# Performance work log

Measured on AMD Instinct MI355X. Metric: run time of the kernel, lower is better.

## Reference

```python
import jax, jax.numpy as jnp
import numpy as np

N, E, DIN, H, C = 50000, 800000, 256, 128, 8


def setup_inputs() -> dict:
    key = jax.random.key(0)
    k1, k2, k3, k4 = jax.random.split(key, 4)
    x = jax.random.normal(k1, (N, DIN), dtype=jnp.float32)
    edge_index = jax.random.randint(k2, (2, E), 0, N, dtype=jnp.int64)
    W1 = jax.random.normal(k3, (DIN, H), dtype=jnp.float32) * (1.0 / np.sqrt(DIN))
    b1 = jnp.zeros((H,), dtype=jnp.float32)
    W2 = jax.random.normal(k4, (H, C), dtype=jnp.float32) * (1.0 / np.sqrt(H))
    b2 = jnp.zeros((C,), dtype=jnp.float32)
    return {"x": x, "W1": W1, "b1": b1, "W2": W2, "b2": b2, "edge_index": edge_index}


def reference(x, W1, b1, W2, b2, edge_index):
    n = x.shape[0]
    loop = jnp.arange(n, dtype=edge_index.dtype)
    src = jnp.concatenate([edge_index[0], loop])  # messages flow src -> dst
    dst = jnp.concatenate([edge_index[1], loop])
    # symmetric GCN normalization with self-loops (PyG GCNConv default)
    deg = jax.ops.segment_sum(jnp.ones_like(dst, dtype=x.dtype), dst, num_segments=n)
    dinv = jnp.where(deg > 0, deg ** -0.5, 0.0)
    norm = dinv[src] * dinv[dst]  # [E+N]

    def gcn_layer(h, W, b):
        h = h @ W                                   # [N, d_out]
        msg = norm[:, None] * h[src]                # gather: [E+N, d_out]
        agg = jax.ops.segment_sum(msg, dst, num_segments=n)  # scatter-add
        return agg + b

    h = jax.nn.relu(gcn_layer(x, W1, b1))
    # F.dropout(training=False) is identity in eval mode
    out = gcn_layer(h, W2, b2)
    return jax.nn.log_softmax(out, axis=1)
```

## Files before the change

kernel.cpp:

```cpp
#include <hip/hip_runtime.h>
#include <hip/hip_bf16.h>
#include <hip/hip_fp16.h>
#include <stdint.h>

#define DIN 256
#define HD  128
#define CD  8
#define KCH 64
#define SBW 72
#define CSRW 64

typedef __attribute__((ext_vector_type(8))) short bf16x8;
typedef __attribute__((ext_vector_type(4))) float f32x4;

__device__ __forceinline__ float bf2f(unsigned short u) {
    union { unsigned int i; float f; } v; v.i = ((unsigned int)u) << 16; return v.f;
}
__device__ __forceinline__ unsigned short f2bf(float f) {
    union { float f; unsigned int i; } v; v.f = f;
    unsigned int r = v.i + 0x7fffu + ((v.i >> 16) & 1u);
    return (unsigned short)(r >> 16);
}
__device__ __forceinline__ int edge_at(const void* ei, int is64, long long idx) {
    return is64 ? (int)((const long long*)ei)[idx] : ((const int*)ei)[idx];
}

__global__ __launch_bounds__(256) void prep_kernel(
    const float* __restrict__ W1, unsigned short* __restrict__ W1T,
    int* __restrict__ count, int N)
{
    int tg = blockIdx.x * 256 + threadIdx.x;
    if (tg < HD * (DIN / 4)) {
        int n  = tg & (HD - 1);
        int k4 = (tg >> 7) * 4;
        unsigned short v[4];
#pragma unroll
        for (int j = 0; j < 4; j++) v[j] = f2bf(W1[(k4 + j) * HD + n]);
        *reinterpret_cast<unsigned long long*>(W1T + (size_t)n * DIN + k4) =
            ((unsigned long long)v[0]) | ((unsigned long long)v[1] << 16) |
            ((unsigned long long)v[2] << 32) | ((unsigned long long)v[3] << 48);
    }
    for (int i = tg; i < N; i += 256 * 256) count[i] = 0;
}

__global__ __launch_bounds__(256) void gemm1_scatter_kernel(
    const float* __restrict__ x, const unsigned short* __restrict__ W1T,
    unsigned short* __restrict__ h, int M,
    const void* __restrict__ ei,
    int* __restrict__ count, unsigned short* __restrict__ colf, int E, int N, int G1)
{
    __shared__ unsigned short w1t[HD * SBW];
    if ((int)blockIdx.x >= G1) {
        const int lane = threadIdx.x & 63;
        int oddw = ((const int*)ei)[2 * lane + 1];
        unsigned long long zb = __ballot(oddw == 0);
        int is64 = (__popcll(zb) >= 56) ? 1 : 0;
        int e0 = ((int)blockIdx.x - G1) * 512 + threadIdx.x;
#pragma unroll
        for (int k = 0; k < 2; k++) {
            int e = e0 + k * 256;
            if (e < E) {
                int s = edge_at(ei, is64, e);
                int d = edge_at(ei, is64, (long long)E + e);
                if ((unsigned)d < (unsigned)N && (unsigned)s < (unsigned)N) {
                    int slot = atomicAdd(&count[d], 1);
                    if (slot < CSRW)
                        colf[(d << 6) + slot] = (unsigned short)s;
                }
            }
        }
        return;
    }
    const int tid  = threadIdx.x;
    const int lane = tid & 63;
    const int wave = tid >> 6;
    const int quad = lane >> 4;
    const int r15  = lane & 15;
    const long long rowBase = (long long)blockIdx.x * 128 + wave * 32;

    f32x4 acc[2][8];
#pragma unroll
    for (int rt = 0; rt < 2; rt++)
#pragma unroll
        for (int ct = 0; ct < 8; ct++)
#pragma unroll
            for (int i = 0; i < 4; i++) acc[rt][ct][i] = 0.0f;

    for (int kh = 0; kh < DIN / KCH; kh++) {
        __syncthreads();
        for (int c = tid; c < HD * (KCH / 8); c += 256) {
            int n   = c >> 3;
            int kk0 = (c & 7) * 8;
            bf16x8 v = *reinterpret_cast<const bf16x8*>(W1T + (size_t)n * DIN + kh * KCH + kk0);
            *reinterpret_cast<bf16x8*>(&w1t[n * SBW + kk0]) = v;
        }
        __syncthreads();

        for (int ki = 0; ki < KCH / 32; ki++) {
            int kk0 = ki * 32 + quad * 8;
            int kg  = kh * KCH + kk0;
            bf16x8 a[2];
#pragma unroll
            for (int rt = 0; rt < 2; rt++) {
                long long row = rowBase + rt * 16 + r15;
                if (row < M) {
                    const float* xp = x + row * DIN + kg;
                    f32x4 f0 = *reinterpret_cast<const f32x4*>(xp);
                    f32x4 f1 = *reinterpret_cast<const f32x4*>(xp + 4);
#pragma unroll
                    for (int j = 0; j < 4; j++) {
                        a[rt][j]     = (short)f2bf(f0[j]);
                        a[rt][j + 4] = (short)f2bf(f1[j]);
                    }
                } else {
#pragma unroll
                    for (int j = 0; j < 8; j++) a[rt][j] = 0;
                }
            }
#pragma unroll
            for (int ct = 0; ct < 8; ct++) {
                bf16x8 b = *reinterpret_cast<const bf16x8*>(&w1t[(ct * 16 + r15) * SBW + kk0]);
                acc[0][ct] = __builtin_amdgcn_mfma_f32_16x16x32_bf16(a[0], b, acc[0][ct], 0, 0, 0);
                acc[1][ct] = __builtin_amdgcn_mfma_f32_16x16x32_bf16(a[1], b, acc[1][ct], 0, 0, 0);
            }
        }
    }
#pragma unroll
    for (int rt = 0; rt < 2; rt++)
#pragma unroll
        for (int ct = 0; ct < 8; ct++)
#pragma unroll
            for (int i = 0; i < 4; i++) {
                long long row = rowBase + rt * 16 + quad * 4 + i;
                if (row < M) h[row * HD + ct * 16 + r15] = f2bf(acc[rt][ct][i]);
            }
}

__global__ __launch_bounds__(256) void scale_kernel(
    const unsigned short* __restrict__ h, const int* __restrict__ count,
    unsigned short* __restrict__ h2, int N)
{
    int t = blockIdx.x * 256 + threadIdx.x;
    if (t >= N * (HD / 8)) return;
    int n = t >> 4;
    int deg = count[n]; if (deg > CSRW) deg = CSRW;
    float dn = rsqrtf((float)deg + 1.0f);
    bf16x8 v = *reinterpret_cast<const bf16x8*>(h + (size_t)t * 8);
    bf16x8 o;
#pragma unroll
    for (int j = 0; j < 8; j++) {
        float f = bf2f((unsigned short)v[j]) * dn;
        __half hf = __float2half(f);
        o[j] = *reinterpret_cast<short*>(&hf);
    }
    *reinterpret_cast<bf16x8*>(h2 + (size_t)t * 8) = o;
}

__global__ __launch_bounds__(256) void agg1_fused_kernel(
    const unsigned short* __restrict__ h2, const int* __restrict__ count,
    const unsigned short* __restrict__ colf, const float* __restrict__ b1,
    const float* __restrict__ W2, float* __restrict__ hw2, int N)
{
    const int lane = threadIdx.x & 63;
    const int n = blockIdx.x * 4 + (threadIdx.x >> 6);
    if (n >= N) return;

    float w2a[CD], w2b[CD];
#pragma unroll
    for (int c = 0; c < CD; c++) {
        w2a[c] = W2[(2 * lane)     * CD + c];
        w2b[c] = W2[(2 * lane + 1) * CD + c];
    }

    int deg = count[n]; if (deg > CSRW) deg = CSRW;
    const float dn = rsqrtf((float)deg + 1.0f);

    union UH { unsigned int u; __half2 h; };
    UH p; p.u = *reinterpret_cast<const unsigned int*>(h2 + ((size_t)n << 7) + 2 * lane);
    float2 pf = __half22float2(p.h);
    float acc0 = pf.x, acc1 = pf.y;

    const int base = n << 6;
    int i = 0;
    for (; i + 7 < deg; i += 8) {
        unsigned long long c0 = *reinterpret_cast<const unsigned long long*>(colf + base + i);
        unsigned long long c1 = *reinterpret_cast<const unsigned long long*>(colf + base + i + 4);
        unsigned int s[8];
#pragma unroll
        for (int j = 0; j < 4; j++) {
            s[j]     = (unsigned int)((c0 >> (16 * j)) & 0xFFFFu);
            s[j + 4] = (unsigned int)((c1 >> (16 * j)) & 0xFFFFu);
        }
        UH hv[8];
#pragma unroll
        for (int j = 0; j < 8; j++)
            hv[j].u = *reinterpret_cast<const unsigned int*>(h2 + ((size_t)s[j] << 7) + 2 * lane);
#pragma unroll
        for (int j = 0; j < 8; j++) {
            float2 f = __half22float2(hv[j].h);
            acc0 += f.x;
            acc1 += f.y;
        }
    }
    for (; i < deg; i++) {
        unsigned int s0 = colf[base + i];
        UH a; a.u = *reinterpret_cast<const unsigned int*>(h2 + ((size_t)s0 << 7) + 2 * lane);
        float2 f = __half22float2(a.h);
        acc0 += f.x;
        acc1 += f.y;
    }

    float v0 = dn * acc0 + b1[2 * lane];     v0 = v0 > 0.0f ? v0 : 0.0f;
    float v1 = dn * acc1 + b1[2 * lane + 1]; v1 = v1 > 0.0f ? v1 : 0.0f;

    float part[CD];
#pragma unroll
    for (int c = 0; c < CD; c++) part[c] = v0 * w2a[c] + v1 * w2b[c];

    float t4[4];
    {
        int hi = lane & 1;
#pragma unroll
        for (int k = 0; k < 4; k++) {
            float send = hi ? part[k] : part[4 + k];
            float recv = __shfl_xor(send, 1, 64);
            t4[k] = (hi ? part[4 + k] : part[k]) + recv;
        }
    }
    float t2[2];
    {
        int hi = (lane >> 1) & 1;
#pragma unroll
        for (int k = 0; k < 2; k++) {
            float send = hi ? t4[k] : t4[2 + k];
            float recv = __shfl_xor(send, 2, 64);
            t2[k] = (hi ? t4[2 + k] : t4[k]) + recv;
        }
    }
    float t1;
    {
        int hi = (lane >> 2) & 1;
        float send = hi ? t2[0] : t2[1];
        float recv = __shfl_xor(send, 4, 64);
        t1 = (hi ? t2[1] : t2[0]) + recv;
    }
    t1 += __shfl_xor(t1, 8, 64);
    t1 += __shfl_xor(t1, 16, 64);
    t1 += __shfl_xor(t1, 32, 64);
    int c = ((lane & 1) << 2) | (lane & 2) | ((lane >> 2) & 1);
    if (lane < CD) hw2[(size_t)n * CD + c] = dn * t1;
}

__global__ __launch_bounds__(256) void agg2_kernel(
    const float* __restrict__ hw2, const int* __restrict__ count,
    const unsigned short* __restrict__ colf, const float* __restrict__ b2,
    float* __restrict__ out, int N) {
    int n = blockIdx.x * 256 + threadIdx.x;
    if (n >= N) return;
    int deg = count[n]; if (deg > CSRW) deg = CSRW;
    float dn = rsqrtf((float)deg + 1.0f);
    f32x4 a0 = *reinterpret_cast<const f32x4*>(hw2 + (size_t)n * CD);
    f32x4 a1 = *reinterpret_cast<const f32x4*>(hw2 + (size_t)n * CD + 4);
    const int base = n << 6;
    int i = 0;
    for (; i + 3 < deg; i += 4) {
        unsigned long long cc = *reinterpret_cast<const unsigned long long*>(colf + base + i);
        unsigned int s0 = (unsigned int)(cc & 0xFFFFu);
        unsigned int s1 = (unsigned int)((cc >> 16) & 0xFFFFu);
        unsigned int s2 = (unsigned int)((cc >> 32) & 0xFFFFu);
        unsigned int s3 = (unsigned int)((cc >> 48) & 0xFFFFu);
        f32x4 b0 = *reinterpret_cast<const f32x4*>(hw2 + (size_t)s0 * CD);
        f32x4 b1 = *reinterpret_cast<const f32x4*>(hw2 + (size_t)s0 * CD + 4);
        f32x4 c0 = *reinterpret_cast<const f32x4*>(hw2 + (size_t)s1 * CD);
        f32x4 c1 = *reinterpret_cast<const f32x4*>(hw2 + (size_t)s1 * CD + 4);
        f32x4 d0 = *reinterpret_cast<const f32x4*>(hw2 + (size_t)s2 * CD);
        f32x4 d1 = *reinterpret_cast<const f32x4*>(hw2 + (size_t)s2 * CD + 4);
        f32x4 e0 = *reinterpret_cast<const f32x4*>(hw2 + (size_t)s3 * CD);
        f32x4 e1 = *reinterpret_cast<const f32x4*>(hw2 + (size_t)s3 * CD + 4);
        a0 += (b0 + c0) + (d0 + e0);
        a1 += (b1 + c1) + (d1 + e1);
    }
    for (; i < deg; i++) {
        unsigned int s0 = colf[base + i];
        a0 += *reinterpret_cast<const f32x4*>(hw2 + (size_t)s0 * CD);
        a1 += *reinterpret_cast<const f32x4*>(hw2 + (size_t)s0 * CD + 4);
    }
    float v[CD];
#pragma unroll
    for (int j = 0; j < 4; j++) {
        v[j]     = dn * a0[j] + b2[j];
        v[4 + j] = dn * a1[j] + b2[4 + j];
    }
    float mx = v[0];
#pragma unroll
    for (int j = 1; j < CD; j++) mx = fmaxf(mx, v[j]);
    float s8 = 0.0f;
#pragma unroll
    for (int j = 0; j < CD; j++) s8 += expf(v[j] - mx);
    float lse = mx + logf(s8);
    f32x4 o0, o1;
#pragma unroll
    for (int j = 0; j < 4; j++) {
        o0[j] = v[j] - lse;
        o1[j] = v[4 + j] - lse;
    }
    *reinterpret_cast<f32x4*>(out + (size_t)n * CD)     = o0;
    *reinterpret_cast<f32x4*>(out + (size_t)n * CD + 4) = o1;
}

extern "C" void kernel_launch(void* const* d_in, const int* in_sizes, int n_in,
                              void* d_out, int out_size, void* d_ws, size_t ws_size,
                              hipStream_t stream) {
    const float* x  = (const float*)d_in[0];
    const float* W1 = (const float*)d_in[1];
    const float* b1 = (const float*)d_in[2];
    const float* W2 = (const float*)d_in[3];
    const float* b2 = (const float*)d_in[4];
    const void*  ei = d_in[5];
    const int N = in_sizes[0] / DIN;
    const int E = in_sizes[5] / 2;
    const int G1 = (N + 127) / 128;
    const int G2 = (E + 511) / 512;

    char* ws = (char*)d_ws;
    size_t off = 0;
    auto alloc = [&](size_t bytes) -> void* {
        void* p = ws + off;
        off = (off + bytes + 255) & ~(size_t)255;
        return p;
    };
    int*   count = (int*)alloc((size_t)N * 4);
    unsigned short* colf = (unsigned short*)alloc((size_t)N * CSRW * 2);
    unsigned short* h = (unsigned short*)alloc((size_t)N * HD * 2);
    unsigned short* h2 = (unsigned short*)alloc((size_t)N * HD * 2);
    float* hw2 = (float*)alloc((size_t)N * CD * 4);
    unsigned short* W1T = (unsigned short*)alloc((size_t)HD * DIN * 2);

    prep_kernel         <<<256, 256, 0, stream>>>(W1, W1T, count, N);
    gemm1_scatter_kernel<<<G1 + G2, 256, 0, stream>>>(x, W1T, h, N, ei, count, colf, E, N, G1);
    scale_kernel        <<<(N * (HD / 8) + 255) / 256, 256, 0, stream>>>(h, count, h2, N);
    agg1_fused_kernel   <<<(N + 3) / 4, 256, 0, stream>>>(h2, count, colf, b1, W2, hw2, N);
    agg2_kernel         <<<(N + 255) / 256, 256, 0, stream>>>(hw2, count, colf, b2,
                                                              (float*)d_out, N);
}
```

Measured before the change: 195.7 us.

## Pad degree counters and split agg1 gather across two half-wave edge streams

```diff
diff --git a/kernel.cpp b/kernel.cpp
--- a/kernel.cpp
+++ b/kernel.cpp
@@ -9,6 +9,7 @@
 #define KCH 64
 #define SBW 72
 #define CSRW 64
+#define CPAD 8
 
 typedef __attribute__((ext_vector_type(8))) short bf16x8;
 typedef __attribute__((ext_vector_type(4))) float f32x4;
@@ -40,7 +41,7 @@
             ((unsigned long long)v[0]) | ((unsigned long long)v[1] << 16) |
             ((unsigned long long)v[2] << 32) | ((unsigned long long)v[3] << 48);
     }
-    for (int i = tg; i < N; i += 256 * 256) count[i] = 0;
+    for (int i = tg; i < N * CPAD; i += 256 * 256) count[i] = 0;
 }
 
 __global__ __launch_bounds__(256) void gemm1_scatter_kernel(
@@ -63,7 +64,7 @@
                 int s = edge_at(ei, is64, e);
                 int d = edge_at(ei, is64, (long long)E + e);
                 if ((unsigned)d < (unsigned)N && (unsigned)s < (unsigned)N) {
-                    int slot = atomicAdd(&count[d], 1);
+                    int slot = atomicAdd(&count[(size_t)d * CPAD], 1);
                     if (slot < CSRW)
                         colf[(d << 6) + slot] = (unsigned short)s;
                 }
@@ -143,7 +144,7 @@
     int t = blockIdx.x * 256 + threadIdx.x;
     if (t >= N * (HD / 8)) return;
     int n = t >> 4;
-    int deg = count[n]; if (deg > CSRW) deg = CSRW;
+    int deg = count[(size_t)n * CPAD]; if (deg > CSRW) deg = CSRW;
     float dn = rsqrtf((float)deg + 1.0f);
     bf16x8 v = *reinterpret_cast<const bf16x8*>(h + (size_t)t * 8);
     bf16x8 o;
@@ -162,60 +163,86 @@
     const float* __restrict__ W2, float* __restrict__ hw2, int N)
 {
     const int lane = threadIdx.x & 63;
+    const int half = lane >> 5;
+    const int l32  = lane & 31;
     const int n = blockIdx.x * 4 + (threadIdx.x >> 6);
     if (n >= N) return;
 
-    float w2a[CD], w2b[CD];
-#pragma unroll
-    for (int c = 0; c < CD; c++) {
-        w2a[c] = W2[(2 * lane)     * CD + c];
-        w2b[c] = W2[(2 * lane + 1) * CD + c];
-    }
-
-    int deg = count[n]; if (deg > CSRW) deg = CSRW;
+    f32x4 w2lo[4], w2hi[4];
+#pragma unroll
+    for (int k = 0; k < 4; k++) {
+        w2lo[k] = *reinterpret_cast<const f32x4*>(W2 + (4 * l32 + k) * CD);
+        w2hi[k] = *reinterpret_cast<const f32x4*>(W2 + (4 * l32 + k) * CD + 4);
+    }
+
+    int deg = count[(size_t)n * CPAD]; if (deg > CSRW) deg = CSRW;
     const float dn = rsqrtf((float)deg + 1.0f);
 
-    union UH { unsigned int u; __half2 h; };
-    UH p; p.u = *reinterpret_cast<const unsigned int*>(h2 + ((size_t)n << 7) + 2 * lane);
-    float2 pf = __half22float2(p.h);
-    float acc0 = pf.x, acc1 = pf.y;
+    union UH4 { uint2 u; __half2 h[2]; };
+    float a0 = 0.0f, a1 = 0.0f, a2 = 0.0f, a3 = 0.0f;
+    if (half == 0) {
+        UH4 p; p.u = *reinterpret_cast<const uint2*>(h2 + ((size_t)n << 7) + 4 * l32);
+        float2 f0 = __half22float2(p.h[0]), f1 = __half22float2(p.h[1]);
+        a0 = f0.x; a1 = f0.y; a2 = f1.x; a3 = f1.y;
+    }
 
     const int base = n << 6;
+    const int sh = 16 * half;
     int i = 0;
     for (; i + 7 < deg; i += 8) {
         unsigned long long c0 = *reinterpret_cast<const unsigned long long*>(colf + base + i);
         unsigned long long c1 = *reinterpret_cast<const unsigned long long*>(colf + base + i + 4);
-        unsigned int s[8];
-#pragma unroll
-        for (int j = 0; j < 4; j++) {
-            s[j]     = (unsigned int)((c0 >> (16 * j)) & 0xFFFFu);
-            s[j + 4] = (unsigned int)((c1 >> (16 * j)) & 0xFFFFu);
-        }
-        UH hv[8];
-#pragma unroll
-        for (int j = 0; j < 8; j++)
-            hv[j].u = *reinterpret_cast<const unsigned int*>(h2 + ((size_t)s[j] << 7) + 2 * lane);
-#pragma unroll
-        for (int j = 0; j < 8; j++) {
-            float2 f = __half22float2(hv[j].h);
-            acc0 += f.x;
-            acc1 += f.y;
-        }
-    }
-    for (; i < deg; i++) {
-        unsigned int s0 = colf[base + i];
-        UH a; a.u = *reinterpret_cast<const unsigned int*>(h2 + ((size_t)s0 << 7) + 2 * lane);
-        float2 f = __half22float2(a.h);
-        acc0 += f.x;
-        acc1 += f.y;
-    }
-
-    float v0 = dn * acc0 + b1[2 * lane];     v0 = v0 > 0.0f ? v0 : 0.0f;
-    float v1 = dn * acc1 + b1[2 * lane + 1]; v1 = v1 > 0.0f ? v1 : 0.0f;
-
+        unsigned int s0 = (unsigned int)((c0 >> sh) & 0xFFFFu);
+        unsigned int s1 = (unsigned int)((c0 >> (32 + sh)) & 0xFFFFu);
+        unsigned int s2 = (unsigned int)((c1 >> sh) & 0xFFFFu);
+        unsigned int s3 = (unsigned int)((c1 >> (32 + sh)) & 0xFFFFu);
+        UH4 v0, v1, v2, v3;
+        v0.u = *reinterpret_cast<const uint2*>(h2 + ((size_t)s0 << 7) + 4 * l32);
+        v1.u = *reinterpret_cast<const uint2*>(h2 + ((size_t)s1 << 7) + 4 * l32);
+        v2.u = *reinterpret_cast<const uint2*>(h2 + ((size_t)s2 << 7) + 4 * l32);
+        v3.u = *reinterpret_cast<const uint2*>(h2 + ((size_t)s3 << 7) + 4 * l32);
+#pragma unroll
+        for (int j = 0; j < 1; j++) {}
+        {
+            float2 f;
+            f = __half22float2(v0.h[0]); a0 += f.x; a1 += f.y;
+            f = __half22float2(v0.h[1]); a2 += f.x; a3 += f.y;
+            f = __half22float2(v1.h[0]); a0 += f.x; a1 += f.y;
+            f = __half22float2(v1.h[1]); a2 += f.x; a3 += f.y;
+            f = __half22float2(v2.h[0]); a0 += f.x; a1 += f.y;
+            f = __half22float2(v2.h[1]); a2 += f.x; a3 += f.y;
+            f = __half22float2(v3.h[0]); a0 += f.x; a1 += f.y;
+            f = __half22float2(v3.h[1]); a2 += f.x; a3 += f.y;
+        }
+    }
+    for (; i + 1 < deg; i += 2) {
+        unsigned int s = colf[base + i + half];
+        UH4 v; v.u = *reinterpret_cast<const uint2*>(h2 + ((size_t)s << 7) + 4 * l32);
+        float2 f0 = __half22float2(v.h[0]), f1 = __half22float2(v.h[1]);
+        a0 += f0.x; a1 += f0.y; a2 += f1.x; a3 += f1.y;
+    }
+    if (i < deg && half == 0) {
+        unsigned int s = colf[base + i];
+        UH4 v; v.u = *reinterpret_cast<const uint2*>(h2 + ((size_t)s << 7) + 4 * l32);
+        float2 f0 = __half22float2(v.h[0]), f1 = __half22float2(v.h[1]);
+        a0 += f0.x; a1 += f0.y; a2 += f1.x; a3 += f1.y;
+    }
+
+    a0 += __shfl_xor(a0, 32, 64);
+    a1 += __shfl_xor(a1, 32, 64);
+    a2 += __shfl_xor(a2, 32, 64);
+    a3 += __shfl_xor(a3, 32, 64);
+
+    float v0 = dn * a0 + b1[4 * l32];     v0 = v0 > 0.0f ? v0 : 0.0f;
+    float v1 = dn * a1 + b1[4 * l32 + 1]; v1 = v1 > 0.0f ? v1 : 0.0f;
+    float v2 = dn * a2 + b1[4 * l32 + 2]; v2 = v2 > 0.0f ? v2 : 0.0f;
+    float v3 = dn * a3 + b1[4 * l32 + 3]; v3 = v3 > 0.0f ? v3 : 0.0f;
+
+    f32x4 plo = v0 * w2lo[0] + v1 * w2lo[1] + v2 * w2lo[2] + v3 * w2lo[3];
+    f32x4 phi = v0 * w2hi[0] + v1 * w2hi[1] + v2 * w2hi[2] + v3 * w2hi[3];
     float part[CD];
 #pragma unroll
-    for (int c = 0; c < CD; c++) part[c] = v0 * w2a[c] + v1 * w2b[c];
+    for (int c = 0; c < 4; c++) { part[c] = plo[c]; part[4 + c] = phi[c]; }
 
     float t4[4];
     {
@@ -246,7 +273,6 @@
     }
     t1 += __shfl_xor(t1, 8, 64);
     t1 += __shfl_xor(t1, 16, 64);
-    t1 += __shfl_xor(t1, 32, 64);
     int c = ((lane & 1) << 2) | (lane & 2) | ((lane >> 2) & 1);
     if (lane < CD) hw2[(size_t)n * CD + c] = dn * t1;
 }
@@ -257,7 +283,7 @@
     float* __restrict__ out, int N) {
     int n = blockIdx.x * 256 + threadIdx.x;
     if (n >= N) return;
-    int deg = count[n]; if (deg > CSRW) deg = CSRW;
+    int deg = count[(size_t)n * CPAD]; if (deg > CSRW) deg = CSRW;
     float dn = rsqrtf((float)deg + 1.0f);
     f32x4 a0 = *reinterpret_cast<const f32x4*>(hw2 + (size_t)n * CD);
     f32x4 a1 = *reinterpret_cast<const f32x4*>(hw2 + (size_t)n * CD + 4);
@@ -270,7 +296,7 @@
         unsigned int s2 = (unsigned int)((cc >> 32) & 0xFFFFu);
         unsigned int s3 = (unsigned int)((cc >> 48) & 0xFFFFu);
         f32x4 b0 = *reinterpret_cast<const f32x4*>(hw2 + (size_t)s0 * CD);
-        f32x4 b1 = *reinterpret_cast<const f32x4*>(hw2 + (size_t)s0 * CD + 4);
+        f32x4 b1v = *reinterpret_cast<const f32x4*>(hw2 + (size_t)s0 * CD + 4);
         f32x4 c0 = *reinterpret_cast<const f32x4*>(hw2 + (size_t)s1 * CD);
         f32x4 c1 = *reinterpret_cast<const f32x4*>(hw2 + (size_t)s1 * CD + 4);
         f32x4 d0 = *reinterpret_cast<const f32x4*>(hw2 + (size_t)s2 * CD);
@@ -278,7 +304,7 @@
         f32x4 e0 = *reinterpret_cast<const f32x4*>(hw2 + (size_t)s3 * CD);
         f32x4 e1 = *reinterpret_cast<const f32x4*>(hw2 + (size_t)s3 * CD + 4);
         a0 += (b0 + c0) + (d0 + e0);
-        a1 += (b1 + c1) + (d1 + e1);
+        a1 += (b1v + c1) + (d1 + e1);
     }
     for (; i < deg; i++) {
         unsigned int s0 = colf[base + i];
@@ -329,7 +355,7 @@
         off = (off + bytes + 255) & ~(size_t)255;
         return p;
     };
-    int*   count = (int*)alloc((size_t)N * 4);
+    int*   count = (int*)alloc((size_t)N * CPAD * 4);
     unsigned short* colf = (unsigned short*)alloc((size_t)N * CSRW * 2);
     unsigned short* h = (unsigned short*)alloc((size_t)N * HD * 2);
     unsigned short* h2 = (unsigned short*)alloc((size_t)N * HD * 2);
```

Result: slower. 235.8 us (+20.5%).
